# Performance work log

Hardware: AMD Instinct MI355X
Metric: run time of the kernel (lower is better)

## Reference

```python
import jax, jax.numpy as jnp
import numpy as np

N = 50000    # nodes
E = 640000   # edges (avg degree ~12.8)
D = 128      # feature dim (input = hidden = output)
L = 3        # num_layers
BN_EPS = 1e-5


def setup_inputs() -> dict:
    key = jax.random.key(0)
    ks = jax.random.split(key, 6)
    x = jax.random.normal(ks[0], (N, D), dtype=jnp.float32)
    edge_index = jax.random.randint(ks[1], (2, E), 0, N, dtype=jnp.int32)
    s = 1.0 / np.sqrt(D)
    # Weights stored as (in, out); equivalent to torch Linear's x @ W.T with W:(out,in).
    W1 = jax.random.normal(ks[2], (L, D, D), dtype=jnp.float32) * s
    b1 = jnp.zeros((L, D), dtype=jnp.float32)
    gamma = jnp.ones((L, D), dtype=jnp.float32)   # BatchNorm weight
    beta = jnp.zeros((L, D), dtype=jnp.float32)   # BatchNorm bias
    W2 = jax.random.normal(ks[3], (L, D, D), dtype=jnp.float32) * s
    b2 = jnp.zeros((L, D), dtype=jnp.float32)
    return {"x": x, "W1": W1, "b1": b1, "gamma": gamma, "beta": beta,
            "W2": W2, "b2": b2, "edge_index": edge_index}


def reference(x, W1, b1, gamma, beta, W2, b2, edge_index):
    src = edge_index[0]
    dst = edge_index[1]
    h = x
    for i in range(L):
        # GINConv aggregation: sum of source-node features into destinations, eps=0
        agg = jax.ops.segment_sum(h[src], dst, num_segments=N)   # [N, D]
        z = h + agg                                              # (1+eps)*x + sum_j x_j
        # MLP: Linear -> BatchNorm1d (training stats) -> ReLU -> Linear
        z = z @ W1[i] + b1[i]
        mu = jnp.mean(z, axis=0)
        var = jnp.mean((z - mu) ** 2, axis=0)                    # biased var (torch BN)
        z = (z - mu) * jax.lax.rsqrt(var + BN_EPS) * gamma[i] + beta[i]
        z = jax.nn.relu(z)
        z = z @ W2[i] + b2[i]
        # inter-layer ReLU (dropout_rate=0 -> identity)
        h = jax.nn.relu(z) if i < L - 1 else z
    return h
```

## Files before the change

kernel.cpp:

```cpp
#include <hip/hip_runtime.h>

#define D 128
#define BN_EPS 1e-5f
#define ELLW 64

typedef __bf16 bf16_t;
typedef __bf16 bf16x8 __attribute__((ext_vector_type(8)));
typedef __bf16 bf16x4 __attribute__((ext_vector_type(4)));
typedef __bf16 bf16x2 __attribute__((ext_vector_type(2)));
typedef float floatx4 __attribute__((ext_vector_type(4)));

__global__ void prep(const float* __restrict__ x, bf16_t* __restrict__ hb,
                     const float* __restrict__ W1, const float* __restrict__ W2,
                     bf16_t* __restrict__ Wsw, int* __restrict__ deg,
                     float* __restrict__ stats, int N, int n4) {
  int i = blockIdx.x * blockDim.x + threadIdx.x;
  if (i < n4) {
    float4 v = ((const float4*)x)[i];
    bf16x4 p;
    p[0] = (bf16_t)v.x; p[1] = (bf16_t)v.y; p[2] = (bf16_t)v.z; p[3] = (bf16_t)v.w;
    *(bf16x4*)(hb + (size_t)4 * i) = p;
  }
  if (i < N) deg[i] = 0;
  if (i < 768) stats[i] = 0.f;
  if (i < 6 * 16384) {
    int mat = i >> 14;
    int kn = i & 16383;
    int k = kn >> 7;
    int n = kn & 127;
    const float* Wm = (mat < 3) ? (W1 + (size_t)mat * 16384)
                                : (W2 + (size_t)(mat - 3) * 16384);
    float v = Wm[kn];
    int f = ((n >> 4) << 2) | (k >> 5);
    int ln = (((k >> 3) & 3) << 4) | (n & 15);
    int j = k & 7;
    Wsw[(size_t)mat * 16384 + ((f << 6) + ln) * 8 + j] = (bf16_t)v;
  }
}

__global__ void ell_fill(const int* __restrict__ src, const int* __restrict__ dst,
                         int* __restrict__ deg, int* __restrict__ ell, int E) {
  int e = blockIdx.x * blockDim.x + threadIdx.x;
  if (e < E) {
    int d = dst[e];
    int slot = atomicAdd(&deg[d], 1);
    if (slot < ELLW) ell[(size_t)d * ELLW + slot] = src[e];
  }
}

__global__ __launch_bounds__(256) void aggregate(
    const bf16_t* __restrict__ h, bf16_t* __restrict__ z,
    const int* __restrict__ ell, const int* __restrict__ deg, int Nn) {
  int node = blockIdx.x * 4 + (threadIdx.x >> 6);
  if (node >= Nn) return;
  int lane = threadIdx.x & 63;
  int off = lane << 1;
  int dg = deg[node]; if (dg > ELLW) dg = ELLW;
  const int* nb = ell + (size_t)node * ELLW;

  bf16x2 sv = *(const bf16x2*)(h + (size_t)node * D + off);
  float a0x = (float)sv[0], a0y = (float)sv[1];
  float a1x = 0.f, a1y = 0.f, a2x = 0.f, a2y = 0.f, a3x = 0.f, a3y = 0.f;
  int e = 0;
  for (; e + 4 <= dg; e += 4) {
    int4 i4 = *(const int4*)(nb + e);
    bf16x2 v0 = *(const bf16x2*)(h + (size_t)i4.x * D + off);
    bf16x2 v1 = *(const bf16x2*)(h + (size_t)i4.y * D + off);
    bf16x2 v2 = *(const bf16x2*)(h + (size_t)i4.z * D + off);
    bf16x2 v3 = *(const bf16x2*)(h + (size_t)i4.w * D + off);
    a0x += (float)v0[0]; a0y += (float)v0[1];
    a1x += (float)v1[0]; a1y += (float)v1[1];
    a2x += (float)v2[0]; a2y += (float)v2[1];
    a3x += (float)v3[0]; a3y += (float)v3[1];
  }
  for (; e < dg; ++e) {
    bf16x2 v = *(const bf16x2*)(h + (size_t)nb[e] * D + off);
    a0x += (float)v[0]; a0y += (float)v[1];
  }
  a0x += a1x + a2x + a3x;
  a0y += a1y + a2y + a3y;
  bf16x2 o;
  o[0] = (bf16_t)a0x; o[1] = (bf16_t)a0y;
  *(bf16x2*)(z + (size_t)node * D + off) = o;
}

__global__ __launch_bounds__(256) void gemm1_stats(
    const bf16_t* __restrict__ Z, const bf16_t* __restrict__ Wsw,
    const float* __restrict__ bias, bf16_t* __restrict__ Yf,
    float* __restrict__ stats, int nStrips, int N) {
  __shared__ bf16_t T[64][136];
  __shared__ float sred[256];
  const int t = threadIdx.x;
  const int wv = t >> 6;
  const int lane = t & 63;
  const int l15 = lane & 15;
  const int quad = lane >> 4;
  const int strip = blockIdx.x * 4 + wv;
  const bool active = strip < nStrips;

  sred[t] = 0.f;

  bf16x8 a[4];
  const int row = strip * 16 + l15;
  if (active && row < N) {
#pragma unroll
    for (int kc = 0; kc < 4; ++kc)
      a[kc] = *(const bf16x8*)(Z + (size_t)row * D + kc * 32 + quad * 8);
  } else {
#pragma unroll
    for (int kc = 0; kc < 4; ++kc)
#pragma unroll
      for (int j = 0; j < 8; ++j) a[kc][j] = (bf16_t)0.f;
  }

  floatx4 acc[8];
#pragma unroll
  for (int nt = 0; nt < 8; ++nt) {
    float bv = bias[nt * 16 + l15];
    acc[nt] = (floatx4){bv, bv, bv, bv};
  }

#pragma unroll
  for (int nt = 0; nt < 8; ++nt) {
#pragma unroll
    for (int kc = 0; kc < 4; ++kc) {
      bf16x8 b = *(const bf16x8*)(Wsw + (size_t)((nt * 4 + kc) * 64 + lane) * 8);
      acc[nt] = __builtin_amdgcn_mfma_f32_16x16x32_bf16(a[kc], b, acc[nt], 0, 0, 0);
    }
  }

  const int lr = wv * 16 + quad * 4;
#pragma unroll
  for (int nt = 0; nt < 8; ++nt) {
    int c = nt * 16 + l15;
#pragma unroll
    for (int r = 0; r < 4; ++r) T[lr + r][c] = (bf16_t)acc[nt][r];
  }
  __syncthreads();
  if (active) {
#pragma unroll
    for (int kc = 0; kc < 4; ++kc) {
      bf16x8 yv = *(const bf16x8*)&T[wv * 16 + l15][kc * 32 + quad * 8];
      *(bf16x8*)(Yf + ((size_t)(strip * 4 + kc) * 64 + lane) * 8) = yv;
    }
  }

  const int rowBase = strip * 16 + quad * 4;
#pragma unroll
  for (int nt = 0; nt < 8; ++nt) {
    int c = nt * 16 + l15;
    float s = 0.f, q = 0.f;
    if (active) {
#pragma unroll
      for (int r = 0; r < 4; ++r) {
        if (rowBase + r < N) {
          float v = acc[nt][r];
          s += v; q += v * v;
        }
      }
    }
    s += __shfl_xor(s, 16); s += __shfl_xor(s, 32);
    q += __shfl_xor(q, 16); q += __shfl_xor(q, 32);
    if (quad == 0) {
      atomicAdd(&sred[c], s);
      atomicAdd(&sred[128 + c], q);
    }
  }
  __syncthreads();
  atomicAdd(&stats[t], sred[t]);
}

__global__ __launch_bounds__(256) void mlp2(
    const bf16_t* __restrict__ Yf, const float* __restrict__ stats,
    const float* __restrict__ gamma, const float* __restrict__ beta,
    const bf16_t* __restrict__ Wsw, const float* __restrict__ bias,
    void* __restrict__ outp, int nStrips, int N, float invN,
    int relu_out, int fp32_out) {
  __shared__ float abL[256];
  const int t = threadIdx.x;
  if (t < 128) {
    float mu = stats[t] * invN;
    float var = fmaxf(stats[128 + t] * invN - mu * mu, 0.f);
    float a = gamma[t] * rsqrtf(var + BN_EPS);
    abL[t] = a;
    abL[128 + t] = beta[t] - mu * a;
  }
  __syncthreads();

  const int wv = t >> 6;
  const int lane = t & 63;
  const int l15 = lane & 15;
  const int quad = lane >> 4;
  const int strip = blockIdx.x * 4 + wv;
  if (strip >= nStrips) return;

  bf16x8 a2[4];
#pragma unroll
  for (int kc = 0; kc < 4; ++kc) {
    bf16x8 y = *(const bf16x8*)(Yf + ((size_t)(strip * 4 + kc) * 64 + lane) * 8);
#pragma unroll
    for (int j = 0; j < 8; ++j) {
      int c = kc * 32 + quad * 8 + j;
      float v = fmaxf(fmaf((float)y[j], abL[c], abL[128 + c]), 0.f);
      a2[kc][j] = (bf16_t)v;
    }
  }

  floatx4 acc[8];
#pragma unroll
  for (int nt = 0; nt < 8; ++nt) {
    float bv = bias[nt * 16 + l15];
    acc[nt] = (floatx4){bv, bv, bv, bv};
  }

#pragma unroll
  for (int nt = 0; nt < 8; ++nt) {
#pragma unroll
    for (int kc = 0; kc < 4; ++kc) {
      bf16x8 b = *(const bf16x8*)(Wsw + (size_t)((nt * 4 + kc) * 64 + lane) * 8);
      acc[nt] = __builtin_amdgcn_mfma_f32_16x16x32_bf16(a2[kc], b, acc[nt], 0, 0, 0);
    }
  }

  const int rowBase = strip * 16 + quad * 4;
  if (fp32_out) {
    float* out = (float*)outp;
#pragma unroll
    for (int nt = 0; nt < 8; ++nt) {
      int c = nt * 16 + l15;
#pragma unroll
      for (int r = 0; r < 4; ++r) {
        int row = rowBase + r;
        if (row < N) {
          float v = acc[nt][r];
          if (relu_out) v = fmaxf(v, 0.f);
          out[(size_t)row * D + c] = v;
        }
      }
    }
  } else {
    bf16_t* out = (bf16_t*)outp;
#pragma unroll
    for (int nt = 0; nt < 8; ++nt) {
      int c = nt * 16 + l15;
#pragma unroll
      for (int r = 0; r < 4; ++r) {
        int row = rowBase + r;
        if (row < N) {
          float v = acc[nt][r];
          if (relu_out) v = fmaxf(v, 0.f);
          out[(size_t)row * D + c] = (bf16_t)v;
        }
      }
    }
  }
}

extern "C" void kernel_launch(void* const* d_in, const int* in_sizes, int n_in,
                              void* d_out, int out_size, void* d_ws, size_t ws_size,
                              hipStream_t stream) {
  const float* x     = (const float*)d_in[0];
  const float* W1    = (const float*)d_in[1];
  const float* b1    = (const float*)d_in[2];
  const float* gamma = (const float*)d_in[3];
  const float* beta  = (const float*)d_in[4];
  const float* W2    = (const float*)d_in[5];
  const float* b2    = (const float*)d_in[6];
  const int*   ei    = (const int*)d_in[7];

  const int N = in_sizes[0] / D;
  const int E = in_sizes[7] / 2;
  const int* src = ei;
  const int* dst = ei + E;
  float* out = (float*)d_out;

  char* ws = (char*)d_ws;
  size_t bufBytes = (size_t)N * D * sizeof(bf16_t);
  bf16_t* hb   = (bf16_t*)ws;
  bf16_t* zb   = (bf16_t*)(ws + bufBytes);
  bf16_t* Yf   = (bf16_t*)(ws + 2 * bufBytes);
  int*    ell  = (int*)(ws + 3 * bufBytes);
  int*    deg  = (int*)((char*)ell + (size_t)N * ELLW * sizeof(int));
  float*  stats = (float*)((char*)deg + (size_t)N * sizeof(int));
  bf16_t* Wsw  = (bf16_t*)((char*)stats + 768 * sizeof(float));

  const int n4 = N * D / 4;
  const int prepBlocks = (n4 + 255) / 256;
  const int eb = (E + 255) / 256;
  const int aggBlocks = (N + 3) / 4;
  const int nStrips = (N + 15) / 16;
  const int gemmBlocks = (nStrips + 3) / 4;
  const float invN = 1.f / (float)N;

  prep<<<prepBlocks, 256, 0, stream>>>(x, hb, W1, W2, Wsw, deg, stats, N, n4);
  ell_fill<<<eb, 256, 0, stream>>>(src, dst, deg, ell, E);

  for (int i = 0; i < 3; ++i) {
    float* st = stats + (size_t)i * 256;
    aggregate<<<aggBlocks, 256, 0, stream>>>(hb, zb, ell, deg, N);
    gemm1_stats<<<gemmBlocks, 256, 0, stream>>>(
        zb, Wsw + (size_t)i * 16384, b1 + (size_t)i * D, Yf, st, nStrips, N);
    void* Ob = (i == 2) ? d_out : (void*)hb;
    mlp2<<<gemmBlocks, 256, 0, stream>>>(
        Yf, st, gamma + (size_t)i * D, beta + (size_t)i * D,
        Wsw + (size_t)(i + 3) * 16384, b2 + (size_t)i * D,
        Ob, nStrips, N, invN, (i < 2) ? 1 : 0, (i == 2) ? 1 : 0);
  }
}
```

Before: 341.9 us.

## Fuse both MLP GEMMs into one kernel with a grid-wide atomic barrier

Merges the first GEMM plus BatchNorm-stats kernel with the second-GEMM kernel. Each block keeps its first-GEMM accumulators in registers, waits on a global atomic counter until every block has added its statistics, then applies BN and ReLU and runs the second GEMM from LDS. This drops the write and reread of the intermediate bf16 activation buffer and one kernel launch per layer. The cost is a spin barrier that depends on all blocks being co-resident (launch bounds set to four blocks per CU), with a timeout guard that would silently let blocks use incomplete statistics.

```diff
diff --git a/kernel.cpp b/kernel.cpp
--- a/kernel.cpp
+++ b/kernel.cpp
@@ -13,7 +13,8 @@
 __global__ void prep(const float* __restrict__ x, bf16_t* __restrict__ hb,
                      const float* __restrict__ W1, const float* __restrict__ W2,
                      bf16_t* __restrict__ Wsw, int* __restrict__ deg,
-                     float* __restrict__ stats, int N, int n4) {
+                     float* __restrict__ stats, unsigned* __restrict__ bar,
+                     int N, int n4) {
   int i = blockIdx.x * blockDim.x + threadIdx.x;
   if (i < n4) {
     float4 v = ((const float4*)x)[i];
@@ -23,6 +24,7 @@
   }
   if (i < N) deg[i] = 0;
   if (i < 768) stats[i] = 0.f;
+  if (i < 4) bar[i] = 0u;
   if (i < 6 * 16384) {
     int mat = i >> 14;
     int kn = i & 16383;
@@ -84,10 +86,14 @@
   *(bf16x2*)(z + (size_t)node * D + off) = o;
 }
 
-__global__ __launch_bounds__(256) void gemm1_stats(
-    const bf16_t* __restrict__ Z, const bf16_t* __restrict__ Wsw,
-    const float* __restrict__ bias, bf16_t* __restrict__ Yf,
-    float* __restrict__ stats, int nStrips, int N) {
+__global__ __launch_bounds__(256, 4) void mlp_fused(
+    const bf16_t* __restrict__ Z, float* __restrict__ stats,
+    const float* __restrict__ gamma, const float* __restrict__ beta,
+    const bf16_t* __restrict__ Wsw1, const float* __restrict__ bias1,
+    const bf16_t* __restrict__ Wsw2, const float* __restrict__ bias2,
+    void* __restrict__ outp, unsigned* __restrict__ bar,
+    int nBlocks, int nStrips, int N, float invN,
+    int relu_out, int fp32_out) {
   __shared__ bf16_t T[64][136];
   __shared__ float sred[256];
   const int t = threadIdx.x;
@@ -116,32 +122,15 @@
   floatx4 acc[8];
 #pragma unroll
   for (int nt = 0; nt < 8; ++nt) {
-    float bv = bias[nt * 16 + l15];
+    float bv = bias1[nt * 16 + l15];
     acc[nt] = (floatx4){bv, bv, bv, bv};
   }
-
 #pragma unroll
   for (int nt = 0; nt < 8; ++nt) {
 #pragma unroll
     for (int kc = 0; kc < 4; ++kc) {
-      bf16x8 b = *(const bf16x8*)(Wsw + (size_t)((nt * 4 + kc) * 64 + lane) * 8);
+      bf16x8 b = *(const bf16x8*)(Wsw1 + (size_t)((nt * 4 + kc) * 64 + lane) * 8);
       acc[nt] = __builtin_amdgcn_mfma_f32_16x16x32_bf16(a[kc], b, acc[nt], 0, 0, 0);
-    }
-  }
-
-  const int lr = wv * 16 + quad * 4;
-#pragma unroll
-  for (int nt = 0; nt < 8; ++nt) {
-    int c = nt * 16 + l15;
-#pragma unroll
-    for (int r = 0; r < 4; ++r) T[lr + r][c] = (bf16_t)acc[nt][r];
-  }
-  __syncthreads();
-  if (active) {
-#pragma unroll
-    for (int kc = 0; kc < 4; ++kc) {
-      bf16x8 yv = *(const bf16x8*)&T[wv * 16 + l15][kc * 32 + quad * 8];
-      *(bf16x8*)(Yf + ((size_t)(strip * 4 + kc) * 64 + lane) * 8) = yv;
     }
   }
 
@@ -168,61 +157,64 @@
   }
   __syncthreads();
   atomicAdd(&stats[t], sred[t]);
-}
-
-__global__ __launch_bounds__(256) void mlp2(
-    const bf16_t* __restrict__ Yf, const float* __restrict__ stats,
-    const float* __restrict__ gamma, const float* __restrict__ beta,
-    const bf16_t* __restrict__ Wsw, const float* __restrict__ bias,
-    void* __restrict__ outp, int nStrips, int N, float invN,
-    int relu_out, int fp32_out) {
-  __shared__ float abL[256];
-  const int t = threadIdx.x;
-  if (t < 128) {
-    float mu = stats[t] * invN;
-    float var = fmaxf(stats[128 + t] * invN - mu * mu, 0.f);
-    float a = gamma[t] * rsqrtf(var + BN_EPS);
-    abL[t] = a;
-    abL[128 + t] = beta[t] - mu * a;
-  }
+
   __syncthreads();
-
-  const int wv = t >> 6;
-  const int lane = t & 63;
-  const int l15 = lane & 15;
-  const int quad = lane >> 4;
-  const int strip = blockIdx.x * 4 + wv;
-  if (strip >= nStrips) return;
+  if (t == 0) {
+    __hip_atomic_fetch_add(bar, 1u, __ATOMIC_RELEASE, __HIP_MEMORY_SCOPE_AGENT);
+    int guard = 0;
+    while (__hip_atomic_load(bar, __ATOMIC_ACQUIRE, __HIP_MEMORY_SCOPE_AGENT)
+           < (unsigned)nBlocks) {
+      __builtin_amdgcn_s_sleep(2);
+      if (++guard > (1 << 22)) break;
+    }
+  }
+  __syncthreads();
+
+  float bnA[8], bnB[8];
+#pragma unroll
+  for (int nt = 0; nt < 8; ++nt) {
+    int c = nt * 16 + l15;
+    float sSum = __hip_atomic_load(&stats[c], __ATOMIC_RELAXED,
+                                   __HIP_MEMORY_SCOPE_AGENT);
+    float qSum = __hip_atomic_load(&stats[128 + c], __ATOMIC_RELAXED,
+                                   __HIP_MEMORY_SCOPE_AGENT);
+    float mu = sSum * invN;
+    float var = fmaxf(qSum * invN - mu * mu, 0.f);
+    float ai = gamma[c] * rsqrtf(var + BN_EPS);
+    bnA[nt] = ai;
+    bnB[nt] = beta[c] - mu * ai;
+  }
+
+  const int lr = wv * 16 + quad * 4;
+#pragma unroll
+  for (int nt = 0; nt < 8; ++nt) {
+    int c = nt * 16 + l15;
+#pragma unroll
+    for (int r = 0; r < 4; ++r)
+      T[lr + r][c] = (bf16_t)fmaxf(fmaf(acc[nt][r], bnA[nt], bnB[nt]), 0.f);
+  }
+  __syncthreads();
 
   bf16x8 a2[4];
 #pragma unroll
-  for (int kc = 0; kc < 4; ++kc) {
-    bf16x8 y = *(const bf16x8*)(Yf + ((size_t)(strip * 4 + kc) * 64 + lane) * 8);
-#pragma unroll
-    for (int j = 0; j < 8; ++j) {
-      int c = kc * 32 + quad * 8 + j;
-      float v = fmaxf(fmaf((float)y[j], abL[c], abL[128 + c]), 0.f);
-      a2[kc][j] = (bf16_t)v;
-    }
-  }
-
-  floatx4 acc[8];
-#pragma unroll
-  for (int nt = 0; nt < 8; ++nt) {
-    float bv = bias[nt * 16 + l15];
+  for (int kc = 0; kc < 4; ++kc)
+    a2[kc] = *(const bf16x8*)&T[wv * 16 + l15][kc * 32 + quad * 8];
+
+#pragma unroll
+  for (int nt = 0; nt < 8; ++nt) {
+    float bv = bias2[nt * 16 + l15];
     acc[nt] = (floatx4){bv, bv, bv, bv};
   }
-
 #pragma unroll
   for (int nt = 0; nt < 8; ++nt) {
 #pragma unroll
     for (int kc = 0; kc < 4; ++kc) {
-      bf16x8 b = *(const bf16x8*)(Wsw + (size_t)((nt * 4 + kc) * 64 + lane) * 8);
+      bf16x8 b = *(const bf16x8*)(Wsw2 + (size_t)((nt * 4 + kc) * 64 + lane) * 8);
       acc[nt] = __builtin_amdgcn_mfma_f32_16x16x32_bf16(a2[kc], b, acc[nt], 0, 0, 0);
     }
   }
 
-  const int rowBase = strip * 16 + quad * 4;
+  if (!active) return;
   if (fp32_out) {
     float* out = (float*)outp;
 #pragma unroll
@@ -230,11 +222,11 @@
       int c = nt * 16 + l15;
 #pragma unroll
       for (int r = 0; r < 4; ++r) {
-        int row = rowBase + r;
-        if (row < N) {
+        int rw = rowBase + r;
+        if (rw < N) {
           float v = acc[nt][r];
           if (relu_out) v = fmaxf(v, 0.f);
-          out[(size_t)row * D + c] = v;
+          out[(size_t)rw * D + c] = v;
         }
       }
     }
@@ -245,11 +237,11 @@
       int c = nt * 16 + l15;
 #pragma unroll
       for (int r = 0; r < 4; ++r) {
-        int row = rowBase + r;
-        if (row < N) {
+        int rw = rowBase + r;
+        if (rw < N) {
           float v = acc[nt][r];
           if (relu_out) v = fmaxf(v, 0.f);
-          out[(size_t)row * D + c] = (bf16_t)v;
+          out[(size_t)rw * D + c] = (bf16_t)v;
         }
       }
     }
@@ -272,17 +264,16 @@
   const int E = in_sizes[7] / 2;
   const int* src = ei;
   const int* dst = ei + E;
-  float* out = (float*)d_out;
 
   char* ws = (char*)d_ws;
   size_t bufBytes = (size_t)N * D * sizeof(bf16_t);
   bf16_t* hb   = (bf16_t*)ws;
   bf16_t* zb   = (bf16_t*)(ws + bufBytes);
-  bf16_t* Yf   = (bf16_t*)(ws + 2 * bufBytes);
   int*    ell  = (int*)(ws + 3 * bufBytes);
   int*    deg  = (int*)((char*)ell + (size_t)N * ELLW * sizeof(int));
   float*  stats = (float*)((char*)deg + (size_t)N * sizeof(int));
-  bf16_t* Wsw  = (bf16_t*)((char*)stats + 768 * sizeof(float));
+  unsigned* bar = (unsigned*)(stats + 768);
+  bf16_t* Wsw  = (bf16_t*)(bar + 4);
 
   const int n4 = N * D / 4;
   const int prepBlocks = (n4 + 255) / 256;
@@ -292,18 +283,18 @@
   const int gemmBlocks = (nStrips + 3) / 4;
   const float invN = 1.f / (float)N;
 
-  prep<<<prepBlocks, 256, 0, stream>>>(x, hb, W1, W2, Wsw, deg, stats, N, n4);
+  prep<<<prepBlocks, 256, 0, stream>>>(x, hb, W1, W2, Wsw, deg, stats, bar, N, n4);
   ell_fill<<<eb, 256, 0, stream>>>(src, dst, deg, ell, E);
 
   for (int i = 0; i < 3; ++i) {
-    float* st = stats + (size_t)i * 256;
     aggregate<<<aggBlocks, 256, 0, stream>>>(hb, zb, ell, deg, N);
-    gemm1_stats<<<gemmBlocks, 256, 0, stream>>>(
-        zb, Wsw + (size_t)i * 16384, b1 + (size_t)i * D, Yf, st, nStrips, N);
     void* Ob = (i == 2) ? d_out : (void*)hb;
-    mlp2<<<gemmBlocks, 256, 0, stream>>>(
-        Yf, st, gamma + (size_t)i * D, beta + (size_t)i * D,
+    mlp_fused<<<gemmBlocks, 256, 0, stream>>>(
+        zb, stats + (size_t)i * 256,
+        gamma + (size_t)i * D, beta + (size_t)i * D,
+        Wsw + (size_t)i * 16384, b1 + (size_t)i * D,
         Wsw + (size_t)(i + 3) * 16384, b2 + (size_t)i * D,
-        Ob, nStrips, N, invN, (i < 2) ? 1 : 0, (i == 2) ? 1 : 0);
-  }
-}
+        Ob, bar + i, gemmBlocks, nStrips, N, invN,
+        (i < 2) ? 1 : 0, (i == 2) ? 1 : 0);
+  }
+}
```

After: 472.0 us. +38.1%, slower.
